# Kernel tuning notes

Hardware: AMD Instinct MI355X
Metric: run time of the kernel (lower is better)

## Reference

```python
import jax, jax.numpy as jnp
import numpy as np

EPS = 1e-5

def conv1x1(x, w):
    # x: [B,C,H,W], w: [O,C] -> [B,O,H,W]
    return jnp.einsum('oc,bchw->bohw', w, x)

def bn(x, g, b, m, v):
    # inference batchnorm over channel dim 1
    scale = g / jnp.sqrt(v + EPS)
    return x * scale[None, :, None, None] + (b - m * scale)[None, :, None, None]

def setup_inputs() -> dict:
    key = jax.random.key(0)
    ks = jax.random.split(key, 20)
    B, Cin, S = 32, 256, 32
    C = Cin // 2
    rn = lambda k, sh: jax.random.normal(k, sh, dtype=jnp.float32)
    ru = lambda k, sh: jax.random.uniform(k, sh, dtype=jnp.float32)
    return {
        'x': rn(ks[0], (B, Cin, S, S)),
        'w1': rn(ks[1], (C, Cin)) * 0.05,
        'bn1_g': ru(ks[2], (C,)) + 0.5,
        'bn1_b': rn(ks[3], (C,)) * 0.1,
        'bn1_m': rn(ks[4], (C,)) * 0.1,
        'bn1_v': ru(ks[5], (C,)) + 0.5,
        'wq': rn(ks[6], (C, C)) * 0.05,
        'bq': rn(ks[7], (C,)) * 0.05,
        'wk': rn(ks[8], (C, C)) * 0.05,
        'bk': rn(ks[9], (C,)) * 0.05,
        'wv': rn(ks[10], (C, C)) * 0.05,
        'bv': rn(ks[11], (C,)) * 0.05,
        'rel_h': rn(ks[12], (1, C, S, 1)),
        'rel_w': rn(ks[13], (1, C, 1, S)),
        'w2': rn(ks[14], (Cin, C)) * 0.05,
        'bn2_g': ru(ks[15], (Cin,)) + 0.5,
        'bn2_b': rn(ks[16], (Cin,)) * 0.1,
        'bn2_m': rn(ks[17], (Cin,)) * 0.1,
        'bn2_v': ru(ks[18], (Cin,)) + 0.5,
    }

def reference(x, w1, bn1_g, bn1_b, bn1_m, bn1_v, wq, bq, wk, bk, wv, bv,
              rel_h, rel_w, w2, bn2_g, bn2_b, bn2_m, bn2_v):
    # cv1: 1x1 conv -> BN -> SiLU
    x1 = jax.nn.silu(bn(conv1x1(x, w1), bn1_g, bn1_b, bn1_m, bn1_v))
    B, C, H, W = x1.shape
    N = H * W
    # q/k/v: 1x1 conv with bias, flattened to [B,C,N]
    q = (conv1x1(x1, wq) + bq[None, :, None, None]).reshape(B, C, N)
    k = (conv1x1(x1, wk) + bk[None, :, None, None]).reshape(B, C, N)
    v = (conv1x1(x1, wv) + bv[None, :, None, None]).reshape(B, C, N)
    # content-content: q^T k -> [B,N,N]
    content_content = jnp.einsum('bci,bcj->bij', q, k)
    # content-position: pos^T q -> [B,N,N]
    pos = (rel_h + rel_w).reshape(C, N)  # [C,N]
    content_position = jnp.einsum('ci,bcj->bij', pos, q)
    attention = jax.nn.softmax(content_content + content_position, axis=-1)
    # out[b,c,i] = sum_j v[b,c,j] * attention[b,i,j]
    out = jnp.einsum('bcj,bij->bci', v, attention).reshape(B, C, H, W)
    # cv2: 1x1 conv -> BN -> SiLU, plus residual shortcut
    y = jax.nn.silu(bn(conv1x1(out, w2), bn2_g, bn2_b, bn2_m, bn2_v))
    return x + y
```

## Files before the change

### kernel.cpp

```cpp
#include <hip/hip_runtime.h>
#include <stdint.h>

typedef __bf16 bf16x8 __attribute__((ext_vector_type(8)));
typedef float  f32x4  __attribute__((ext_vector_type(4)));

#define MFMA(a,b,c)   __builtin_amdgcn_mfma_f32_16x16x32_bf16((a),(b),(c),0,0,0)

__device__ __forceinline__ short f2b(float x) {
  uint32_t u = __float_as_uint(x);
  uint32_t r = (u + 0x7fffu + ((u >> 16) & 1u)) >> 16;
  return (short)r;
}

__device__ __forceinline__ void glds16(const void* g, void* l) {
  __builtin_amdgcn_global_load_lds(
      (const __attribute__((address_space(1))) void*)(uintptr_t)g,
      (__attribute__((address_space(3))) void*)(uintptr_t)l, 16, 0, 0);
}

__global__ void k_prep(const float* __restrict__ w1, const float* __restrict__ wq,
                       const float* __restrict__ wk, const float* __restrict__ wv,
                       const float* __restrict__ w2,
                       const float* __restrict__ relh, const float* __restrict__ relw,
                       const float* __restrict__ g1, const float* __restrict__ b1,
                       const float* __restrict__ m1, const float* __restrict__ v1,
                       const float* __restrict__ g2, const float* __restrict__ b2,
                       const float* __restrict__ m2, const float* __restrict__ v2,
                       short* __restrict__ w1b, short* __restrict__ wqb,
                       short* __restrict__ wkb, short* __restrict__ wvb,
                       short* __restrict__ w2b, short* __restrict__ posT,
                       float* __restrict__ bnc) {
  int i = blockIdx.x * 256 + threadIdx.x;
  if (i < 32768) { w1b[i] = f2b(w1[i]); return; }
  i -= 32768;
  if (i < 16384) { wqb[i] = f2b(wq[i]); return; }
  i -= 16384;
  if (i < 16384) { wkb[i] = f2b(wk[i]); return; }
  i -= 16384;
  if (i < 16384) { wvb[i] = f2b(wv[i]); return; }
  i -= 16384;
  if (i < 32768) { w2b[i] = f2b(w2[i]); return; }
  i -= 32768;
  if (i < 131072) {
    int n = i >> 7, c = i & 127;
    int h = n >> 5, w = n & 31;
    posT[i] = f2b(relh[c * 32 + h] + relw[c * 32 + w]);
    return;
  }
  i -= 131072;
  if (i < 128) { float s = g1[i] * rsqrtf(v1[i] + 1e-5f); bnc[i] = s; bnc[128 + i] = b1[i] - m1[i] * s; return; }
  i -= 128;
  if (i < 256) { float s = g2[i] * rsqrtf(v2[i] + 1e-5f); bnc[256 + i] = s; bnc[512 + i] = b2[i] - m2[i] * s; return; }
}

__launch_bounds__(256)
__global__ void k_cq(const float* __restrict__ x, const short* __restrict__ w1b,
                     const short* __restrict__ wqb, const short* __restrict__ wkb,
                     const short* __restrict__ wvb, const float* __restrict__ bnc,
                     const float* __restrict__ bq, const float* __restrict__ bk,
                     const float* __restrict__ bv,
                     short* __restrict__ qT, short* __restrict__ kT,
                     short* __restrict__ vv) {
  __shared__ __align__(16) short Al[128 * 40];
  __shared__ __align__(16) short Bl[128 * 40];
  __shared__ __align__(16) short X1[128 * 136];
  const int bx = blockIdx.x;
  const int b = bx >> 3;
  const int n0 = (bx & 7) << 7;
  const int tid = threadIdx.x;
  const int wid = tid >> 6, lane = tid & 63;
  const int wr = wid >> 1, wc = wid & 1;
  const int cpr = lane & 15, g = lane >> 4;
  const float* xb = x + (size_t)b * (256 * 1024);

  {
    f32x4 acc[4][4] = {};
    for (int kk = 0; kk < 8; ++kk) {
#pragma unroll
      for (int it = 0; it < 2; ++it) {
        int f = tid + it * 256;
        int row = f >> 2, c8 = f & 3;
        *reinterpret_cast<uint4*>(&Al[row * 40 + c8 * 8]) =
            *reinterpret_cast<const uint4*>(&w1b[row * 256 + kk * 32 + c8 * 8]);
      }
#pragma unroll
      for (int it = 0; it < 4; ++it) {
        int f = tid + it * 256;
        int ci = f >> 5, c4 = f & 31;
        float4 v4 = *reinterpret_cast<const float4*>(&xb[(size_t)(kk * 32 + ci) * 1024 + n0 + c4 * 4]);
        int nb = c4 * 4;
        Bl[(nb + 0) * 40 + ci] = f2b(v4.x);
        Bl[(nb + 1) * 40 + ci] = f2b(v4.y);
        Bl[(nb + 2) * 40 + ci] = f2b(v4.z);
        Bl[(nb + 3) * 40 + ci] = f2b(v4.w);
      }
      __syncthreads();
      bf16x8 af[4], bfr[4];
#pragma unroll
      for (int mf = 0; mf < 4; ++mf)
        af[mf] = *reinterpret_cast<const bf16x8*>(&Al[(wr * 64 + mf * 16 + cpr) * 40 + g * 8]);
#pragma unroll
      for (int nf = 0; nf < 4; ++nf)
        bfr[nf] = *reinterpret_cast<const bf16x8*>(&Bl[(wc * 64 + nf * 16 + cpr) * 40 + g * 8]);
#pragma unroll
      for (int mf = 0; mf < 4; ++mf)
#pragma unroll
        for (int nf = 0; nf < 4; ++nf)
          acc[mf][nf] = MFMA(af[mf], bfr[nf], acc[mf][nf]);
      __syncthreads();
    }
#pragma unroll
    for (int mf = 0; mf < 4; ++mf) {
      int m0 = wr * 64 + mf * 16 + g * 4;
#pragma unroll
      for (int nf = 0; nf < 4; ++nf) {
        int nl = wc * 64 + nf * 16 + cpr;
        union { short s[4]; uint2 u; } pk;
#pragma unroll
        for (int r = 0; r < 4; ++r) {
          int c = m0 + r;
          float z = acc[mf][nf][r] * bnc[c] + bnc[128 + c];
          pk.s[r] = f2b(z / (1.f + __expf(-z)));
        }
        *reinterpret_cast<uint2*>(&X1[nl * 136 + m0]) = pk.u;
      }
    }
  }
  __syncthreads();

  for (int which = 0; which < 3; ++which) {
    const short* W = which == 0 ? wqb : which == 1 ? wkb : wvb;
    const float* bias = which == 0 ? bq : which == 1 ? bk : bv;
    f32x4 acc[4][4] = {};
    for (int kk = 0; kk < 4; ++kk) {
#pragma unroll
      for (int it = 0; it < 2; ++it) {
        int f = tid + it * 256;
        int row = f >> 2, c8 = f & 3;
        *reinterpret_cast<uint4*>(&Al[row * 40 + c8 * 8]) =
            *reinterpret_cast<const uint4*>(&W[row * 128 + kk * 32 + c8 * 8]);
      }
      __syncthreads();
      bf16x8 af[4], bfr[4];
#pragma unroll
      for (int mf = 0; mf < 4; ++mf)
        af[mf] = *reinterpret_cast<const bf16x8*>(&Al[(wr * 64 + mf * 16 + cpr) * 40 + g * 8]);
#pragma unroll
      for (int nf = 0; nf < 4; ++nf)
        bfr[nf] = *reinterpret_cast<const bf16x8*>(&X1[(wc * 64 + nf * 16 + cpr) * 136 + kk * 32 + g * 8]);
#pragma unroll
      for (int mf = 0; mf < 4; ++mf)
#pragma unroll
        for (int nf = 0; nf < 4; ++nf)
          acc[mf][nf] = MFMA(af[mf], bfr[nf], acc[mf][nf]);
      __syncthreads();
    }
#pragma unroll
    for (int mf = 0; mf < 4; ++mf) {
      int m0 = wr * 64 + mf * 16 + g * 4;
#pragma unroll
      for (int nf = 0; nf < 4; ++nf) {
        int n = n0 + wc * 64 + nf * 16 + cpr;
        if (which < 2) {
          union { short s4[4]; uint2 u; } pk;
#pragma unroll
          for (int r = 0; r < 4; ++r)
            pk.s4[r] = f2b(acc[mf][nf][r] + bias[m0 + r]);
          short* dst = which == 0 ? qT : kT;
          *reinterpret_cast<uint2*>(&dst[((size_t)b * 1024 + n) * 128 + m0]) = pk.u;
        } else {
#pragma unroll
          for (int r = 0; r < 4; ++r) {
            int c = m0 + r;
            vv[((size_t)b * 128 + c) * 1024 + n] = f2b(acc[mf][nf][r] + bias[c]);
          }
        }
      }
    }
  }
}

__launch_bounds__(512, 2)
__global__ void k_attn(const short* __restrict__ qT, const short* __restrict__ kT,
                       const short* __restrict__ vv, const short* __restrict__ posT,
                       short* __restrict__ oT) {
  __shared__ __align__(16) char smem[98304];
  short* KhB0 = (short*)smem;
  short* KhB1 = (short*)(smem + 32768);
  short* VtB0 = (short*)(smem + 65536);
  short* VtB1 = (short*)(smem + 65536 + 16384);
  float* Obuf = (float*)smem;
  float* mlf  = (float*)(smem + 65536);

  const int bx0 = blockIdx.x;
  const int lbx = ((bx0 & 7) << 5) | (bx0 >> 3);
  const int b  = lbx >> 3;
  const int i0 = (lbx & 7) << 7;
  const int tid = threadIdx.x;
  const int wid = tid >> 6, lane = tid & 63;
  const int rl = lane & 31, hi = lane >> 5;
  const int jh = wid >> 2, iq = wid & 3;
  const size_t bN = (size_t)b * 1024;

  const short* srcK[4];
  const short* srcV[2];
#pragma unroll
  for (int it = 0; it < 4; ++it) {
    int gq = it * 512 + tid;
    int row = gq >> 5, p = gq & 31;
    int l = p ^ (row & 7);
    srcK[it] = (l < 16) ? &kT[(bN + row) * 128 + l * 8]
                        : &qT[(bN + row) * 128 + (l - 16) * 8];
  }
#pragma unroll
  for (int it = 0; it < 2; ++it) {
    int gq = it * 512 + tid;
    int c = gq >> 3, p = gq & 7;
    int l = p ^ (c & 7);
    srcV[it] = &vv[((size_t)b * 128 + c) * 1024 + l * 8];
  }
#pragma unroll
  for (int it = 0; it < 4; ++it) glds16(srcK[it], &KhB0[(it * 512 + wid * 64) * 8]);
#pragma unroll
  for (int it = 0; it < 2; ++it) glds16(srcV[it], &VtB0[(it * 512 + wid * 64) * 8]);

  typedef float f32x16v __attribute__((ext_vector_type(16)));
  bf16x8 qf[16];
  {
    const int irow = i0 + iq * 32 + rl;
#pragma unroll
    for (int ks = 0; ks < 8; ++ks)
      qf[ks] = *reinterpret_cast<const bf16x8*>(&qT[(bN + irow) * 128 + ks * 16 + hi * 8]);
#pragma unroll
    for (int ks = 8; ks < 16; ++ks)
      qf[ks] = *reinterpret_cast<const bf16x8*>(&posT[(size_t)irow * 128 + (ks - 8) * 16 + hi * 8]);
  }
  __syncthreads();

  f32x16v oacc[4] = {};
  float mrow = -3e38f, lrow = 0.f;

  for (int jt = 0; jt < 16; ++jt) {
    const int cur = jt & 1;
    if (jt < 15) {
      short* KhN = cur ? KhB0 : KhB1;
      short* VtN = cur ? VtB0 : VtB1;
#pragma unroll
      for (int it = 0; it < 4; ++it)
        glds16(srcK[it] + ((jt + 1) << 13), &KhN[(it * 512 + wid * 64) * 8]);
#pragma unroll
      for (int it = 0; it < 2; ++it)
        glds16(srcV[it] + ((jt + 1) << 6), &VtN[(it * 512 + wid * 64) * 8]);
    }
    const short* KhC = cur ? KhB1 : KhB0;
    const short* VtC = cur ? VtB1 : VtB0;

    f32x16v s0 = {}, s1 = {};
    {
      const int rb = (jh * 32 + rl) * 256;
      __builtin_amdgcn_s_setprio(1);
#pragma unroll
      for (int ks = 0; ks < 16; ++ks) {
        int p = ((ks << 1) | hi) ^ (rl & 7);
        bf16x8 kf = *reinterpret_cast<const bf16x8*>(&KhC[rb + p * 8]);
        if (ks & 1) s1 = __builtin_amdgcn_mfma_f32_32x32x16_bf16(kf, qf[ks], s1, 0, 0, 0);
        else        s0 = __builtin_amdgcn_mfma_f32_32x32x16_bf16(kf, qf[ks], s0, 0, 0, 0);
      }
      __builtin_amdgcn_s_setprio(0);
    }
    float t[16];
#pragma unroll
    for (int r = 0; r < 16; ++r) t[r] = s0[r] + s1[r];
    float mx = t[0];
#pragma unroll
    for (int r = 1; r < 16; ++r) mx = fmaxf(mx, t[r]);
    mx = fmaxf(mx, __shfl_xor(mx, 32));
    float mnew = fmaxf(mrow, mx);
    float sc = __expf(mrow - mnew);
    float ps = 0.f;
    float pr[16];
#pragma unroll
    for (int r = 0; r < 16; ++r) { pr[r] = __expf(t[r] - mnew); ps += pr[r]; }
    ps += __shfl_xor(ps, 32);
    lrow = lrow * sc + ps;
    mrow = mnew;
#pragma unroll
    for (int ct = 0; ct < 4; ++ct)
#pragma unroll
      for (int r = 0; r < 16; ++r) oacc[ct][r] *= sc;
    uint32_t own[8], rcv[8];
#pragma unroll
    for (int idx = 0; idx < 8; ++idx) {
      uint32_t w;
      asm("v_cvt_pk_bf16_f32 %0, %1, %2" : "=v"(w) : "v"(pr[2 * idx]), "v"(pr[2 * idx + 1]));
      own[idx] = w;
    }
#pragma unroll
    for (int idx = 0; idx < 8; ++idx) rcv[idx] = __shfl_xor((int)own[idx], 32);
#pragma unroll
    for (int js = 0; js < 2; ++js) {
      union { uint32_t u[4]; bf16x8 v; } pa;
      pa.u[0] = hi ? rcv[4 * js + 2] : own[4 * js + 0];
      pa.u[1] = hi ? rcv[4 * js + 3] : own[4 * js + 1];
      pa.u[2] = hi ? own[4 * js + 2] : rcv[4 * js + 0];
      pa.u[3] = hi ? own[4 * js + 3] : rcv[4 * js + 1];
      __builtin_amdgcn_s_setprio(1);
#pragma unroll
      for (int ct = 0; ct < 4; ++ct) {
        int c = ct * 32 + rl;
        int p = ((jh << 2) | (js << 1) | hi) ^ (rl & 7);
        bf16x8 vf = *reinterpret_cast<const bf16x8*>(&VtC[c * 64 + p * 8]);
        oacc[ct] = __builtin_amdgcn_mfma_f32_32x32x16_bf16(vf, pa.v, oacc[ct], 0, 0, 0);
      }
      __builtin_amdgcn_s_setprio(0);
    }
    __syncthreads();
  }

  if (lane < 32) {
    mlf[wid * 64 + rl]      = mrow;
    mlf[wid * 64 + 32 + rl] = lrow;
  }
  __syncthreads();
  {
    const int pid = wid ^ 4;
    float mp = mlf[pid * 64 + rl];
    float lp = mlf[pid * 64 + 32 + rl];
    float M  = fmaxf(mrow, mp);
    float f  = __expf(mrow - M);
    float fp = __expf(mp - M);
    float L  = lrow * f + lp * fp;
    float scl = f / L;
    __syncthreads();
    if (jh == 0) {
#pragma unroll
      for (int ct = 0; ct < 4; ++ct)
#pragma unroll
        for (int r = 0; r < 16; ++r) {
          int creg = (r & 3) + 8 * (r >> 2) + 4 * hi;
          Obuf[iq * 4096 + (ct * 32 + creg) * 32 + rl] = oacc[ct][r] * scl;
        }
    }
    __syncthreads();
    if (jh == 1) {
#pragma unroll
      for (int ct = 0; ct < 4; ++ct)
#pragma unroll
        for (int r = 0; r < 16; ++r) {
          int creg = (r & 3) + 8 * (r >> 2) + 4 * hi;
          Obuf[iq * 4096 + (ct * 32 + creg) * 32 + rl] += oacc[ct][r] * scl;
        }
    }
  }
  __syncthreads();
#pragma unroll
  for (int it = 0; it < 4; ++it) {
    int idx = it * 512 + tid;
    int ig = idx & 127, oct = idx >> 7;
    int iq2 = ig >> 5, il2 = ig & 31;
    union { short s8[8]; uint4 u; } pk8;
#pragma unroll
    for (int e = 0; e < 8; ++e)
      pk8.s8[e] = f2b(Obuf[iq2 * 4096 + (oct * 8 + e) * 32 + il2]);
    *reinterpret_cast<uint4*>(&oT[(bN + i0 + ig) * 128 + oct * 8]) = pk8.u;
  }
}

__launch_bounds__(256)
__global__ void k_conv2(const float* __restrict__ x, const short* __restrict__ w2b,
                        const short* __restrict__ oT, const float* __restrict__ bnc,
                        float* __restrict__ out) {
  __shared__ __align__(16) short Al[128 * 40];
  __shared__ __align__(16) short Bl[128 * 40];
  const int bx = blockIdx.x;
  const int b = bx >> 4;
  const int mt = (bx >> 3) & 1;
  const int n0 = (bx & 7) << 7;
  const int tid = threadIdx.x;
  const int wid = tid >> 6, lane = tid & 63;
  const int wr = wid >> 1, wc = wid & 1;
  const int cpr = lane & 15, g = lane >> 4;
  f32x4 acc[4][4] = {};
  for (int kk = 0; kk < 4; ++kk) {
#pragma unroll
    for (int it = 0; it < 2; ++it) {
      int f = tid + it * 256;
      int row = f >> 2, c8 = f & 3;
      *reinterpret_cast<uint4*>(&Al[row * 40 + c8 * 8]) =
          *reinterpret_cast<const uint4*>(&w2b[(size_t)(mt * 128 + row) * 128 + kk * 32 + c8 * 8]);
      *reinterpret_cast<uint4*>(&Bl[row * 40 + c8 * 8]) =
          *reinterpret_cast<const uint4*>(&oT[((size_t)b * 1024 + n0 + row) * 128 + kk * 32 + c8 * 8]);
    }
    __syncthreads();
    bf16x8 af[4], bfr[4];
#pragma unroll
    for (int mf = 0; mf < 4; ++mf)
      af[mf] = *reinterpret_cast<const bf16x8*>(&Al[(wr * 64 + mf * 16 + cpr) * 40 + g * 8]);
#pragma unroll
    for (int nf = 0; nf < 4; ++nf)
      bfr[nf] = *reinterpret_cast<const bf16x8*>(&Bl[(wc * 64 + nf * 16 + cpr) * 40 + g * 8]);
#pragma unroll
    for (int mf = 0; mf < 4; ++mf)
#pragma unroll
      for (int nf = 0; nf < 4; ++nf)
        acc[mf][nf] = MFMA(af[mf], bfr[nf], acc[mf][nf]);
    __syncthreads();
  }
#pragma unroll
  for (int mf = 0; mf < 4; ++mf) {
    int m0 = wr * 64 + mf * 16 + g * 4;
#pragma unroll
    for (int nf = 0; nf < 4; ++nf) {
      int n = n0 + wc * 64 + nf * 16 + cpr;
#pragma unroll
      for (int r = 0; r < 4; ++r) {
        int co = mt * 128 + m0 + r;
        float z = acc[mf][nf][r];
        float y = z * bnc[256 + co] + bnc[512 + co];
        float sl = y / (1.f + __expf(-y));
        size_t idx = ((size_t)b * 256 + co) * 1024 + n;
        out[idx] = x[idx] + sl;
      }
    }
  }
}

extern "C" void kernel_launch(void* const* d_in, const int* in_sizes, int n_in,
                              void* d_out, int out_size, void* d_ws, size_t ws_size,
                              hipStream_t stream) {
  (void)in_sizes; (void)n_in; (void)out_size; (void)ws_size;
  const float* x    = (const float*)d_in[0];
  const float* w1   = (const float*)d_in[1];
  const float* g1   = (const float*)d_in[2];
  const float* b1   = (const float*)d_in[3];
  const float* m1   = (const float*)d_in[4];
  const float* v1   = (const float*)d_in[5];
  const float* wq   = (const float*)d_in[6];
  const float* bq   = (const float*)d_in[7];
  const float* wk   = (const float*)d_in[8];
  const float* bk   = (const float*)d_in[9];
  const float* wv   = (const float*)d_in[10];
  const float* bv   = (const float*)d_in[11];
  const float* relh = (const float*)d_in[12];
  const float* relw = (const float*)d_in[13];
  const float* w2   = (const float*)d_in[14];
  const float* g2   = (const float*)d_in[15];
  const float* b2   = (const float*)d_in[16];
  const float* m2   = (const float*)d_in[17];
  const float* v2   = (const float*)d_in[18];
  float* out = (float*)d_out;

  char* ws = (char*)d_ws;
  const size_t OFF_W1B  = 0;
  const size_t OFF_WQB  = 65536;
  const size_t OFF_WKB  = 98304;
  const size_t OFF_WVB  = 131072;
  const size_t OFF_W2B  = 163840;
  const size_t OFF_POST = 229376;
  const size_t OFF_BN   = 491520;
  const size_t OFF_OT   = 494592;
  const size_t OFF_QT   = OFF_OT + 8388608;
  const size_t OFF_KT   = OFF_QT + 8388608;
  const size_t OFF_V    = OFF_KT + 8388608;

  short* w1b  = (short*)(ws + OFF_W1B);
  short* wqb  = (short*)(ws + OFF_WQB);
  short* wkb  = (short*)(ws + OFF_WKB);
  short* wvb  = (short*)(ws + OFF_WVB);
  short* w2b  = (short*)(ws + OFF_W2B);
  short* posT = (short*)(ws + OFF_POST);
  float* bnc  = (float*)(ws + OFF_BN);
  short* qT   = (short*)(ws + OFF_QT);
  short* kT   = (short*)(ws + OFF_KT);
  short* vv   = (short*)(ws + OFF_V);
  short* oT   = (short*)(ws + OFF_OT);

  k_prep<<<962, 256, 0, stream>>>(w1, wq, wk, wv, w2, relh, relw,
                                  g1, b1, m1, v1, g2, b2, m2, v2,
                                  w1b, wqb, wkb, wvb, w2b, posT, bnc);
  k_cq<<<256, 256, 0, stream>>>(x, w1b, wqb, wkb, wvb, bnc, bq, bk, bv, qT, kT, vv);
  k_attn<<<256, 512, 0, stream>>>(qT, kT, vv, posT, oT);
  k_conv2<<<512, 256, 0, stream>>>(x, w2b, oT, bnc, out);
}
```

Before: 104.7 us.

## Fuse conv2+BN+SiLU+residual epilogue into attention kernel and skip rescale

The separate conv2 kernel is folded into the attention kernel's epilogue. The merged attention output is converted to bf16 in swizzled LDS and multiplied by w2 with 32x32 MFMAs, then BN, SiLU and the residual add are applied, so the oT round trip to global memory and one launch go away. The online softmax also skips the max update and accumulator rescale when the new tile max stays within 8 of the running max, which saves exp and multiply work per tile. Launch bounds drop to one block per CU because LDS grows, which may reduce overlap.

```diff
diff --git a/kernel.cpp b/kernel.cpp
--- a/kernel.cpp
+++ b/kernel.cpp
@@ -3,13 +3,21 @@
 
 typedef __bf16 bf16x8 __attribute__((ext_vector_type(8)));
 typedef float  f32x4  __attribute__((ext_vector_type(4)));
+typedef float  f32x16 __attribute__((ext_vector_type(16)));
 
 #define MFMA(a,b,c)   __builtin_amdgcn_mfma_f32_16x16x32_bf16((a),(b),(c),0,0,0)
+#define MFMA32(a,b,c) __builtin_amdgcn_mfma_f32_32x32x16_bf16((a),(b),(c),0,0,0)
 
 __device__ __forceinline__ short f2b(float x) {
   uint32_t u = __float_as_uint(x);
   uint32_t r = (u + 0x7fffu + ((u >> 16) & 1u)) >> 16;
   return (short)r;
+}
+
+__device__ __forceinline__ uint32_t cvtpk(float lo, float hi) {
+  uint32_t w;
+  asm("v_cvt_pk_bf16_f32 %0, %1, %2" : "=v"(w) : "v"(lo), "v"(hi));
+  return w;
 }
 
 __device__ __forceinline__ void glds16(const void* g, void* l) {
@@ -180,17 +188,19 @@
   }
 }
 
-__launch_bounds__(512, 2)
+__launch_bounds__(512, 1)
 __global__ void k_attn(const short* __restrict__ qT, const short* __restrict__ kT,
                        const short* __restrict__ vv, const short* __restrict__ posT,
-                       short* __restrict__ oT) {
-  __shared__ __align__(16) char smem[98304];
+                       const short* __restrict__ w2b, const float* __restrict__ bnc,
+                       const float* __restrict__ x, float* __restrict__ out) {
+  __shared__ __align__(16) char smem[100864];
   short* KhB0 = (short*)smem;
   short* KhB1 = (short*)(smem + 32768);
   short* VtB0 = (short*)(smem + 65536);
   short* VtB1 = (short*)(smem + 65536 + 16384);
-  float* Obuf = (float*)smem;
-  float* mlf  = (float*)(smem + 65536);
+  float*    Obuf  = (float*)smem;
+  uint16_t* ObufB = (uint16_t*)(smem + 66048);
+  float*    mlf   = (float*)(smem + 98816);
 
   const int bx0 = blockIdx.x;
   const int lbx = ((bx0 & 7) << 5) | (bx0 >> 3);
@@ -224,7 +234,6 @@
 #pragma unroll
   for (int it = 0; it < 2; ++it) glds16(srcV[it], &VtB0[(it * 512 + wid * 64) * 8]);
 
-  typedef float f32x16v __attribute__((ext_vector_type(16)));
   bf16x8 qf[16];
   {
     const int irow = i0 + iq * 32 + rl;
@@ -237,7 +246,7 @@
   }
   __syncthreads();
 
-  f32x16v oacc[4] = {};
+  f32x16 oacc[4] = {};
   float mrow = -3e38f, lrow = 0.f;
 
   for (int jt = 0; jt < 16; ++jt) {
@@ -255,7 +264,7 @@
     const short* KhC = cur ? KhB1 : KhB0;
     const short* VtC = cur ? VtB1 : VtB0;
 
-    f32x16v s0 = {}, s1 = {};
+    f32x16 s0 = {}, s1 = {};
     {
       const int rb = (jh * 32 + rl) * 256;
       __builtin_amdgcn_s_setprio(1);
@@ -263,8 +272,8 @@
       for (int ks = 0; ks < 16; ++ks) {
         int p = ((ks << 1) | hi) ^ (rl & 7);
         bf16x8 kf = *reinterpret_cast<const bf16x8*>(&KhC[rb + p * 8]);
-        if (ks & 1) s1 = __builtin_amdgcn_mfma_f32_32x32x16_bf16(kf, qf[ks], s1, 0, 0, 0);
-        else        s0 = __builtin_amdgcn_mfma_f32_32x32x16_bf16(kf, qf[ks], s0, 0, 0, 0);
+        if (ks & 1) s1 = MFMA32(kf, qf[ks], s1);
+        else        s0 = MFMA32(kf, qf[ks], s0);
       }
       __builtin_amdgcn_s_setprio(0);
     }
@@ -275,26 +284,29 @@
 #pragma unroll
     for (int r = 1; r < 16; ++r) mx = fmaxf(mx, t[r]);
     mx = fmaxf(mx, __shfl_xor(mx, 32));
-    float mnew = fmaxf(mrow, mx);
-    float sc = __expf(mrow - mnew);
+    float pr[16];
     float ps = 0.f;
-    float pr[16];
-#pragma unroll
-    for (int r = 0; r < 16; ++r) { pr[r] = __expf(t[r] - mnew); ps += pr[r]; }
-    ps += __shfl_xor(ps, 32);
-    lrow = lrow * sc + ps;
-    mrow = mnew;
-#pragma unroll
-    for (int ct = 0; ct < 4; ++ct)
-#pragma unroll
-      for (int r = 0; r < 16; ++r) oacc[ct][r] *= sc;
+    if (__all(mx <= mrow + 8.f)) {
+#pragma unroll
+      for (int r = 0; r < 16; ++r) { pr[r] = __expf(t[r] - mrow); ps += pr[r]; }
+      ps += __shfl_xor(ps, 32);
+      lrow += ps;
+    } else {
+      float mnew = fmaxf(mrow, mx);
+      float sc = __expf(mrow - mnew);
+#pragma unroll
+      for (int r = 0; r < 16; ++r) { pr[r] = __expf(t[r] - mnew); ps += pr[r]; }
+      ps += __shfl_xor(ps, 32);
+      lrow = lrow * sc + ps;
+      mrow = mnew;
+#pragma unroll
+      for (int ct = 0; ct < 4; ++ct)
+#pragma unroll
+        for (int r = 0; r < 16; ++r) oacc[ct][r] *= sc;
+    }
     uint32_t own[8], rcv[8];
 #pragma unroll
-    for (int idx = 0; idx < 8; ++idx) {
-      uint32_t w;
-      asm("v_cvt_pk_bf16_f32 %0, %1, %2" : "=v"(w) : "v"(pr[2 * idx]), "v"(pr[2 * idx + 1]));
-      own[idx] = w;
-    }
+    for (int idx = 0; idx < 8; ++idx) own[idx] = cvtpk(pr[2 * idx], pr[2 * idx + 1]);
 #pragma unroll
     for (int idx = 0; idx < 8; ++idx) rcv[idx] = __shfl_xor((int)own[idx], 32);
 #pragma unroll
@@ -310,7 +322,7 @@
         int c = ct * 32 + rl;
         int p = ((jh << 2) | (js << 1) | hi) ^ (rl & 7);
         bf16x8 vf = *reinterpret_cast<const bf16x8*>(&VtC[c * 64 + p * 8]);
-        oacc[ct] = __builtin_amdgcn_mfma_f32_32x32x16_bf16(vf, pa.v, oacc[ct], 0, 0, 0);
+        oacc[ct] = MFMA32(vf, pa.v, oacc[ct]);
       }
       __builtin_amdgcn_s_setprio(0);
     }
@@ -322,6 +334,7 @@
     mlf[wid * 64 + 32 + rl] = lrow;
   }
   __syncthreads();
+  float scl;
   {
     const int pid = wid ^ 4;
     float mp = mlf[pid * 64 + rl];
@@ -329,98 +342,74 @@
     float M  = fmaxf(mrow, mp);
     float f  = __expf(mrow - M);
     float fp = __expf(mp - M);
-    float L  = lrow * f + lp * fp;
-    float scl = f / L;
-    __syncthreads();
-    if (jh == 0) {
-#pragma unroll
-      for (int ct = 0; ct < 4; ++ct)
-#pragma unroll
-        for (int r = 0; r < 16; ++r) {
-          int creg = (r & 3) + 8 * (r >> 2) + 4 * hi;
-          Obuf[iq * 4096 + (ct * 32 + creg) * 32 + rl] = oacc[ct][r] * scl;
-        }
-    }
-    __syncthreads();
-    if (jh == 1) {
-#pragma unroll
-      for (int ct = 0; ct < 4; ++ct)
-#pragma unroll
-        for (int r = 0; r < 16; ++r) {
-          int creg = (r & 3) + 8 * (r >> 2) + 4 * hi;
-          Obuf[iq * 4096 + (ct * 32 + creg) * 32 + rl] += oacc[ct][r] * scl;
-        }
-    }
-  }
-  __syncthreads();
+    scl = f / (lrow * f + lp * fp);
+  }
+  bf16x8 af2[8];
+#pragma unroll
+  for (int ks = 0; ks < 8; ++ks)
+    af2[ks] = *reinterpret_cast<const bf16x8*>(&w2b[(size_t)(wid * 32 + rl) * 128 + ks * 16 + hi * 8]);
+  __syncthreads();
+
+  const int row = iq * 32 + rl;
+  if (jh == 0) {
+#pragma unroll
+    for (int ct = 0; ct < 4; ++ct)
+#pragma unroll
+      for (int r = 0; r < 16; ++r) {
+        int c = ct * 32 + (r & 3) + 8 * (r >> 2) + 4 * hi;
+        Obuf[row * 129 + c] = oacc[ct][r] * scl;
+      }
+  }
+  __syncthreads();
+  if (jh == 1) {
+    uint32_t* OW = (uint32_t*)ObufB;
+#pragma unroll
+    for (int ct = 0; ct < 4; ++ct) {
+      float mg[16];
+#pragma unroll
+      for (int r = 0; r < 16; ++r) {
+        int c = ct * 32 + (r & 3) + 8 * (r >> 2) + 4 * hi;
+        mg[r] = Obuf[row * 129 + c] + oacc[ct][r] * scl;
+      }
+#pragma unroll
+      for (int m = 0; m < 8; ++m) {
+        int c0 = ct * 32 + ((2 * m) & 3) + 8 * ((2 * m) >> 2) + 4 * hi;
+        int gI = c0 >> 3, wo = (c0 & 7) >> 1;
+        int gS = gI ^ (row & 15);
+        OW[row * 64 + gS * 4 + wo] = cvtpk(mg[2 * m], mg[2 * m + 1]);
+      }
+    }
+  }
+  __syncthreads();
+
+  f32x16 a2[4] = {};
 #pragma unroll
   for (int it = 0; it < 4; ++it) {
-    int idx = it * 512 + tid;
-    int ig = idx & 127, oct = idx >> 7;
-    int iq2 = ig >> 5, il2 = ig & 31;
-    union { short s8[8]; uint4 u; } pk8;
-#pragma unroll
-    for (int e = 0; e < 8; ++e)
-      pk8.s8[e] = f2b(Obuf[iq2 * 4096 + (oct * 8 + e) * 32 + il2]);
-    *reinterpret_cast<uint4*>(&oT[(bN + i0 + ig) * 128 + oct * 8]) = pk8.u;
-  }
-}
-
-__launch_bounds__(256)
-__global__ void k_conv2(const float* __restrict__ x, const short* __restrict__ w2b,
-                        const short* __restrict__ oT, const float* __restrict__ bnc,
-                        float* __restrict__ out) {
-  __shared__ __align__(16) short Al[128 * 40];
-  __shared__ __align__(16) short Bl[128 * 40];
-  const int bx = blockIdx.x;
-  const int b = bx >> 4;
-  const int mt = (bx >> 3) & 1;
-  const int n0 = (bx & 7) << 7;
-  const int tid = threadIdx.x;
-  const int wid = tid >> 6, lane = tid & 63;
-  const int wr = wid >> 1, wc = wid & 1;
-  const int cpr = lane & 15, g = lane >> 4;
-  f32x4 acc[4][4] = {};
-  for (int kk = 0; kk < 4; ++kk) {
-#pragma unroll
-    for (int it = 0; it < 2; ++it) {
-      int f = tid + it * 256;
-      int row = f >> 2, c8 = f & 3;
-      *reinterpret_cast<uint4*>(&Al[row * 40 + c8 * 8]) =
-          *reinterpret_cast<const uint4*>(&w2b[(size_t)(mt * 128 + row) * 128 + kk * 32 + c8 * 8]);
-      *reinterpret_cast<uint4*>(&Bl[row * 40 + c8 * 8]) =
-          *reinterpret_cast<const uint4*>(&oT[((size_t)b * 1024 + n0 + row) * 128 + kk * 32 + c8 * 8]);
-    }
-    __syncthreads();
-    bf16x8 af[4], bfr[4];
-#pragma unroll
-    for (int mf = 0; mf < 4; ++mf)
-      af[mf] = *reinterpret_cast<const bf16x8*>(&Al[(wr * 64 + mf * 16 + cpr) * 40 + g * 8]);
-#pragma unroll
-    for (int nf = 0; nf < 4; ++nf)
-      bfr[nf] = *reinterpret_cast<const bf16x8*>(&Bl[(wc * 64 + nf * 16 + cpr) * 40 + g * 8]);
-#pragma unroll
-    for (int mf = 0; mf < 4; ++mf)
-#pragma unroll
-      for (int nf = 0; nf < 4; ++nf)
-        acc[mf][nf] = MFMA(af[mf], bfr[nf], acc[mf][nf]);
-    __syncthreads();
-  }
-#pragma unroll
-  for (int mf = 0; mf < 4; ++mf) {
-    int m0 = wr * 64 + mf * 16 + g * 4;
-#pragma unroll
-    for (int nf = 0; nf < 4; ++nf) {
-      int n = n0 + wc * 64 + nf * 16 + cpr;
-#pragma unroll
-      for (int r = 0; r < 4; ++r) {
-        int co = mt * 128 + m0 + r;
-        float z = acc[mf][nf][r];
-        float y = z * bnc[256 + co] + bnc[512 + co];
-        float sl = y / (1.f + __expf(-y));
-        size_t idx = ((size_t)b * 256 + co) * 1024 + n;
-        out[idx] = x[idx] + sl;
-      }
+    const int r2 = it * 32 + rl;
+    __builtin_amdgcn_s_setprio(1);
+#pragma unroll
+    for (int ks = 0; ks < 8; ++ks) {
+      int gS = ((ks << 1) | hi) ^ (r2 & 15);
+      bf16x8 bf = *reinterpret_cast<const bf16x8*>(&ObufB[r2 * 128 + gS * 8]);
+      a2[it] = MFMA32(af2[ks], bf, a2[it]);
+    }
+    __builtin_amdgcn_s_setprio(0);
+  }
+  float bsc[16], bsh[16];
+#pragma unroll
+  for (int r = 0; r < 16; ++r) {
+    int co = wid * 32 + (r & 3) + 8 * (r >> 2) + 4 * hi;
+    bsc[r] = bnc[256 + co];
+    bsh[r] = bnc[512 + co];
+  }
+#pragma unroll
+  for (int it = 0; it < 4; ++it) {
+#pragma unroll
+    for (int r = 0; r < 16; ++r) {
+      int co = wid * 32 + (r & 3) + 8 * (r >> 2) + 4 * hi;
+      size_t idx = ((size_t)b * 256 + co) * 1024 + i0 + it * 32 + rl;
+      float y = a2[it][r] * bsc[r] + bsh[r];
+      out[idx] = x[idx] + y / (1.f + __expf(-y));
     }
   }
 }
@@ -458,8 +447,7 @@
   const size_t OFF_W2B  = 163840;
   const size_t OFF_POST = 229376;
   const size_t OFF_BN   = 491520;
-  const size_t OFF_OT   = 494592;
-  const size_t OFF_QT   = OFF_OT + 8388608;
+  const size_t OFF_QT   = 494592;
   const size_t OFF_KT   = OFF_QT + 8388608;
   const size_t OFF_V    = OFF_KT + 8388608;
 
@@ -473,12 +461,10 @@
   short* qT   = (short*)(ws + OFF_QT);
   short* kT   = (short*)(ws + OFF_KT);
   short* vv   = (short*)(ws + OFF_V);
-  short* oT   = (short*)(ws + OFF_OT);
 
   k_prep<<<962, 256, 0, stream>>>(w1, wq, wk, wv, w2, relh, relw,
                                   g1, b1, m1, v1, g2, b2, m2, v2,
                                   w1b, wqb, wkb, wvb, w2b, posT, bnc);
   k_cq<<<256, 256, 0, stream>>>(x, w1b, wqb, wkb, wvb, bnc, bq, bk, bv, qT, kT, vv);
-  k_attn<<<256, 512, 0, stream>>>(qT, kT, vv, posT, oT);
-  k_conv2<<<512, 256, 0, stream>>>(x, w2b, oT, bnc, out);
-}
+  k_attn<<<256, 512, 0, stream>>>(qT, kT, vv, posT, w2b, bnc, x, out);
+}
```

After: 97.13 us, median of 2. 1.08x faster.
